# Kernel tuning notes

Measured on AMD Instinct MI355X. Metric: run time of the kernel, lower is better.

## Reference

```python
import jax, jax.numpy as jnp
import numpy as np

N = 4096  # seq len, used for cos/sin positional reweighting


def _non_neg(x):
    # exp(x) for x<0, x+1 for x>=0
    return jnp.where(x < 0, jnp.exp(x), x + 1.0)


def setup_inputs() -> dict:
    key = jax.random.key(0)
    kq, kk, kv = jax.random.split(key, 3)
    shape = (4, 16, N, 64)
    q = jax.random.normal(kq, shape, dtype=jnp.float32)
    k = jax.random.normal(kk, shape, dtype=jnp.float32)
    v = jax.random.normal(kv, shape, dtype=jnp.float32)
    return {"q": q, "k": k, "v": v}


def reference(q, k, v):
    s = q.shape[-2]
    pos = (jnp.pi / 2.0 / s) * jnp.arange(s, dtype=q.dtype)
    cos = jnp.cos(pos)[:, None]  # [S, 1], broadcasts over feature dim
    sin = jnp.sin(pos)[:, None]
    qf = _non_neg(q)
    kf = _non_neg(k)
    q_cos, q_sin = qf * cos, qf * sin  # [B, H, S, D]
    k_cos, k_sin = kf * cos, kf * sin
    # O(N) kv aggregation: [B, H, D, Dv]
    kv_cos = jnp.einsum('bhsd,bhse->bhde', k_cos, v)
    kv_sin = jnp.einsum('bhsd,bhse->bhde', k_sin, v)
    out = jnp.einsum('bhsd,bhde->bhse', q_cos, kv_cos) + \
          jnp.einsum('bhsd,bhde->bhse', q_sin, kv_sin)
    return out
```

## Files before the change

### kernel.cpp

```cpp
#include <hip/hip_runtime.h>
#include <math.h>

#define SLEN 4096
#define DH   64
#define BHN  64
#define CH   16
#define ROWSPER 256
#define NT   4
#define SPAD 72

typedef float  f32x4  __attribute__((ext_vector_type(4)));
typedef short  s16x4  __attribute__((ext_vector_type(4)));
typedef __bf16 bf16x8 __attribute__((ext_vector_type(8)));

static constexpr float ANG  = 1.5707963267948966f / 4096.0f;
static constexpr float C1   = 0.9999999264657180f;
static constexpr float S1   = 3.8349518757139556e-4f;
static constexpr float ROTC = 0.9996988186962042f;
static constexpr float ROTS = 0.024541228522912288f;

static __device__ __forceinline__ float featf(float x) {
    return x < 0.f ? __expf(x) : x + 1.f;
}
static __device__ __forceinline__ void pack2(short* p, float a, float b) {
    union { __bf16 h[2]; unsigned u; } uu;
    uu.h[0] = (__bf16)a; uu.h[1] = (__bf16)b;
    *(unsigned*)p = uu.u;
}
static __device__ __forceinline__ float b2f(short s) {
    unsigned u = ((unsigned)(unsigned short)s) << 16;
    float f; __builtin_memcpy(&f, &u, 4); return f;
}
static __device__ __forceinline__ short f2b(float f) {
    __bf16 h = (__bf16)f; short s; __builtin_memcpy(&s, &h, 2); return s;
}

__global__ __launch_bounds__(256) void kv_partial(const float* __restrict__ k,
                                                  const float* __restrict__ v,
                                                  short* __restrict__ part)
{
    __shared__ short kcT[64 * SPAD];
    __shared__ short ksT[64 * SPAD];
    __shared__ short vT [64 * SPAD];

    const int bx = blockIdx.x;
    const int bh = bx >> 4, ch = bx & 15;
    const size_t base = (size_t)bh * SLEN * DH;
    const int t  = threadIdx.x;
    const int wv = t >> 6;
    const int ln = t & 63;
    const int m  = ln & 15;
    const int g  = ln >> 4;
    const int d0 = (t & 15) * 4;
    const int sg = t >> 4;
    const int srow_base = ch * ROWSPER;

    float cA[2], sA[2], cB[2], sB[2];
    #pragma unroll
    for (int it = 0; it < 2; ++it) {
        float sn, cs;
        __sincosf(ANG * (float)(srow_base + it * 32 + sg * 2), &sn, &cs);
        cA[it] = cs;            sA[it] = sn;
        cB[it] = cs * C1 - sn * S1;
        sB[it] = sn * C1 + cs * S1;
    }

    f32x4 aC[4] = {}; f32x4 aS[4] = {};
    f32x4 K0[2][2], K1[2][2], V0[2][2], V1[2][2];

#define LOADT(BUF, TILE)                                                      \
    _Pragma("unroll")                                                         \
    for (int it = 0; it < 2; ++it) {                                          \
        const size_t r = base + (size_t)(srow_base + (TILE) * 64 + it * 32 + sg * 2) * DH + d0; \
        K0[BUF][it] = *(const f32x4*)&k[r];                                   \
        K1[BUF][it] = *(const f32x4*)&k[r + DH];                              \
        V0[BUF][it] = *(const f32x4*)&v[r];                                   \
        V1[BUF][it] = *(const f32x4*)&v[r + DH];                              \
    }

    LOADT(0, 0);

    #pragma unroll
    for (int tile = 0; tile < NT; ++tile) {
        const int buf = tile & 1;
        if (tile) __syncthreads();
        #pragma unroll
        for (int it = 0; it < 2; ++it) {
            const int sl = it * 32 + sg * 2;
            #pragma unroll
            for (int i = 0; i < 4; ++i) {
                const int d  = d0 + i;
                const float kf0 = featf(K0[buf][it][i]);
                const float kf1 = featf(K1[buf][it][i]);
                const int pos = ((((sl >> 3) ^ ((d >> 2) & 7)) << 3) | (sl & 7));
                const int ro  = d * SPAD + pos;
                pack2(&kcT[ro], kf0 * cA[it], kf1 * cB[it]);
                pack2(&ksT[ro], kf0 * sA[it], kf1 * sB[it]);
                pack2(&vT [ro], V0[buf][it][i], V1[buf][it][i]);
            }
        }
        __syncthreads();
        if (tile + 1 < NT) { LOADT(buf ^ 1, tile + 1); }
        #pragma unroll
        for (int it = 0; it < 2; ++it) {
            float c = cA[it], s = sA[it];
            cA[it] = c * ROTC - s * ROTS; sA[it] = s * ROTC + c * ROTS;
            c = cB[it]; s = sB[it];
            cB[it] = c * ROTC - s * ROTS; sB[it] = s * ROTC + c * ROTS;
        }
        #pragma unroll
        for (int b = 0; b < 2; ++b) {
            const int s3 = b * 4 + g;
            const int dA = wv * 16 + m;
            const int oA = dA * SPAD + ((s3 ^ ((dA >> 2) & 7)) << 3);
            const bf16x8 Ac = *(const bf16x8*)&kcT[oA];
            const bf16x8 As = *(const bf16x8*)&ksT[oA];
            #pragma unroll
            for (int nt = 0; nt < 4; ++nt) {
                const int dB = nt * 16 + m;
                const int oB = dB * SPAD + ((s3 ^ ((dB >> 2) & 7)) << 3);
                const bf16x8 Bv = *(const bf16x8*)&vT[oB];
                aC[nt] = __builtin_amdgcn_mfma_f32_16x16x32_bf16(Ac, Bv, aC[nt], 0, 0, 0);
                aS[nt] = __builtin_amdgcn_mfma_f32_16x16x32_bf16(As, Bv, aS[nt], 0, 0, 0);
            }
        }
    }
#undef LOADT

    const size_t pb = (size_t)bx * 8192;
    #pragma unroll
    for (int nt = 0; nt < 4; ++nt) {
        #pragma unroll
        for (int r = 0; r < 4; ++r) {
            const int rowb = (wv * 16 + g * 4 + r) * 64 + nt * 16 + m;
            part[pb        + rowb] = f2b(aC[nt][r]);
            part[pb + 4096 + rowb] = f2b(aS[nt][r]);
        }
    }
}

__global__ __launch_bounds__(256) void kv_reduce(const short* __restrict__ part,
                                                 short* __restrict__ kvT)
{
    const int bx = blockIdx.x;
    const int bh = bx >> 3, seg = bx & 7;
    const size_t pbase = (size_t)bh * CH * 8192;
    const int j0 = seg * 1024 + threadIdx.x * 4;
    float acc[4] = {};
    #pragma unroll
    for (int c = 0; c < CH; ++c) {
        const s16x4 sv = *(const s16x4*)&part[pbase + (size_t)c * 8192 + j0];
        #pragma unroll
        for (int i = 0; i < 4; ++i) acc[i] += b2f(sv[i]);
    }
    const int cs = j0 >> 12;
    const int d  = (j0 >> 6) & 63;
    const int e0 = j0 & 63;
    #pragma unroll
    for (int i = 0; i < 4; ++i)
        kvT[(size_t)bh * 8192 + cs * 4096 + (e0 + i) * 64 + d] = f2b(acc[i]);
}

__global__ __launch_bounds__(256) void out_kernel(const float* __restrict__ q,
                                                  const short* __restrict__ kvT,
                                                  float* __restrict__ out)
{
    const int bx = blockIdx.x;
    const int bh = bx >> 4, chunk = bx & 15;
    const int t = threadIdx.x;
    const int wv = t >> 6, ln = t & 63, m = ln & 15, g = ln >> 4;
    const size_t qbase = (size_t)bh * SLEN * DH;
    const size_t kvb   = (size_t)bh * 8192;

    bf16x8 Bc[4][2], Bs[4][2];
    #pragma unroll
    for (int nt = 0; nt < 4; ++nt)
        #pragma unroll
        for (int b = 0; b < 2; ++b) {
            const int off = (nt * 16 + m) * 64 + b * 32 + g * 8;
            Bc[nt][b] = *(const bf16x8*)&kvT[kvb + off];
            Bs[nt][b] = *(const bf16x8*)&kvT[kvb + 4096 + off];
        }

    const int sA = chunk * 256 + wv * 16 + m;
    f32x4 qb[4], qn[4];
    #pragma unroll
    for (int p = 0; p < 4; ++p)
        qb[p] = *(const f32x4*)&q[qbase + (size_t)sA * DH + (p >> 1) * 32 + g * 8 + (p & 1) * 4];

    for (int it = 0; it < 4; ++it) {
        const int srow = sA + it * 64;
        if (it < 3) {
            #pragma unroll
            for (int p = 0; p < 4; ++p)
                qn[p] = *(const f32x4*)&q[qbase + (size_t)(srow + 64) * DH + (p >> 1) * 32 + g * 8 + (p & 1) * 4];
        }
        float sn, c;
        __sincosf(ANG * (float)srow, &sn, &c);
        union { bf16x8 v; __bf16 e[8]; } Ac[2], As[2];
        #pragma unroll
        for (int p = 0; p < 4; ++p) {
            #pragma unroll
            for (int i = 0; i < 4; ++i) {
                const float qf = featf(qb[p][i]);
                Ac[p >> 1].e[(p & 1) * 4 + i] = (__bf16)(qf * c);
                As[p >> 1].e[(p & 1) * 4 + i] = (__bf16)(qf * sn);
            }
        }
        f32x4 acc[4] = {};
        #pragma unroll
        for (int nt = 0; nt < 4; ++nt) {
            acc[nt] = __builtin_amdgcn_mfma_f32_16x16x32_bf16(Ac[0].v, Bc[nt][0], acc[nt], 0, 0, 0);
            acc[nt] = __builtin_amdgcn_mfma_f32_16x16x32_bf16(Ac[1].v, Bc[nt][1], acc[nt], 0, 0, 0);
            acc[nt] = __builtin_amdgcn_mfma_f32_16x16x32_bf16(As[0].v, Bs[nt][0], acc[nt], 0, 0, 0);
            acc[nt] = __builtin_amdgcn_mfma_f32_16x16x32_bf16(As[1].v, Bs[nt][1], acc[nt], 0, 0, 0);
        }
        const int s0 = chunk * 256 + (it * 4 + wv) * 16;
        #pragma unroll
        for (int r = 0; r < 4; ++r) {
            const size_t ob = ((size_t)bh * SLEN + s0 + g * 4 + r) * 64;
            #pragma unroll
            for (int nt = 0; nt < 4; ++nt)
                out[ob + nt * 16 + m] = acc[nt][r];
        }
        if (it < 3) {
            #pragma unroll
            for (int p = 0; p < 4; ++p) qb[p] = qn[p];
        }
    }
}

extern "C" void kernel_launch(void* const* d_in, const int* in_sizes, int n_in,
                              void* d_out, int out_size, void* d_ws, size_t ws_size,
                              hipStream_t stream) {
    const float* q = (const float*)d_in[0];
    const float* k = (const float*)d_in[1];
    const float* v = (const float*)d_in[2];
    float* out  = (float*)d_out;
    short* part = (short*)d_ws;
    short* kvT  = (short*)((char*)d_ws + (size_t)BHN * CH * 8192 * 2);

    hipLaunchKernelGGL(kv_partial, dim3(BHN * CH), dim3(256), 0, stream, k, v, part);
    hipLaunchKernelGGL(kv_reduce,  dim3(BHN * 8),  dim3(256), 0, stream, part, kvT);
    hipLaunchKernelGGL(out_kernel, dim3(BHN * 16), dim3(256), 0, stream, q, kvT, out);
}
```

Before: 66.83 us.

## Feed 32x32x16 MFMA operands directly from global loads, dropping LDS staging

The kv_partial kernel no longer transposes K features and V into shared memory. Each lane loads 8 strided scalar rows of k and v straight into registers, builds bf16 MFMA operands in place, and issues 32x32x16 bf16 MFMAs. Each wave covers a 32x32 quadrant of the D x Dv output. The goal is to remove the LDS writes and reads and the block barriers. In exchange, global loads become scalar 4-byte accesses, and each row of k and v is loaded by two waves, which may hurt memory coalescing. Cos/sin are now advanced by a per-step rotation plus small per-row constant tables.

```diff
diff --git a/kernel.cpp b/kernel.cpp
--- a/kernel.cpp
+++ b/kernel.cpp
@@ -6,26 +6,16 @@
 #define BHN  64
 #define CH   16
 #define ROWSPER 256
-#define NT   4
-#define SPAD 72
-
-typedef float  f32x4  __attribute__((ext_vector_type(4)));
-typedef short  s16x4  __attribute__((ext_vector_type(4)));
-typedef __bf16 bf16x8 __attribute__((ext_vector_type(8)));
-
-static constexpr float ANG  = 1.5707963267948966f / 4096.0f;
-static constexpr float C1   = 0.9999999264657180f;
-static constexpr float S1   = 3.8349518757139556e-4f;
-static constexpr float ROTC = 0.9996988186962042f;
-static constexpr float ROTS = 0.024541228522912288f;
+
+typedef float  f32x4   __attribute__((ext_vector_type(4)));
+typedef float  f32x16  __attribute__((ext_vector_type(16)));
+typedef short  s16x4   __attribute__((ext_vector_type(4)));
+typedef __bf16 bf16x8  __attribute__((ext_vector_type(8)));
+
+static constexpr float ANG = 3.8349519697141029e-4f;
 
 static __device__ __forceinline__ float featf(float x) {
     return x < 0.f ? __expf(x) : x + 1.f;
-}
-static __device__ __forceinline__ void pack2(short* p, float a, float b) {
-    union { __bf16 h[2]; unsigned u; } uu;
-    uu.h[0] = (__bf16)a; uu.h[1] = (__bf16)b;
-    *(unsigned*)p = uu.u;
 }
 static __device__ __forceinline__ float b2f(short s) {
     unsigned u = ((unsigned)(unsigned short)s) << 16;
@@ -39,103 +29,73 @@
                                                   const float* __restrict__ v,
                                                   short* __restrict__ part)
 {
-    __shared__ short kcT[64 * SPAD];
-    __shared__ short ksT[64 * SPAD];
-    __shared__ short vT [64 * SPAD];
+    static constexpr float CJ[8] = {
+        1.0f, 0.999999926470f, 0.9999997058633f, 0.9999993381923f,
+        0.9999988234532f, 0.9999981616455f, 0.9999973527695f, 0.9999963968250f};
+    static constexpr float SJ[8] = {
+        0.0f, 3.83495188e-4f, 7.66990319e-4f, 1.15048534e-3f,
+        1.53398019e-3f, 1.91747481e-3f, 2.30096915e-3f, 2.68446316e-3f};
+    static constexpr float RC16 = 0.99998117528260111f;
+    static constexpr float RS16 = 6.1358846491544753e-3f;
 
     const int bx = blockIdx.x;
     const int bh = bx >> 4, ch = bx & 15;
     const size_t base = (size_t)bh * SLEN * DH;
     const int t  = threadIdx.x;
-    const int wv = t >> 6;
-    const int ln = t & 63;
-    const int m  = ln & 15;
-    const int g  = ln >> 4;
-    const int d0 = (t & 15) * 4;
-    const int sg = t >> 4;
-    const int srow_base = ch * ROWSPER;
-
-    float cA[2], sA[2], cB[2], sB[2];
-    #pragma unroll
-    for (int it = 0; it < 2; ++it) {
-        float sn, cs;
-        __sincosf(ANG * (float)(srow_base + it * 32 + sg * 2), &sn, &cs);
-        cA[it] = cs;            sA[it] = sn;
-        cB[it] = cs * C1 - sn * S1;
-        sB[it] = sn * C1 + cs * S1;
-    }
-
-    f32x4 aC[4] = {}; f32x4 aS[4] = {};
-    f32x4 K0[2][2], K1[2][2], V0[2][2], V1[2][2];
-
-#define LOADT(BUF, TILE)                                                      \
-    _Pragma("unroll")                                                         \
-    for (int it = 0; it < 2; ++it) {                                          \
-        const size_t r = base + (size_t)(srow_base + (TILE) * 64 + it * 32 + sg * 2) * DH + d0; \
-        K0[BUF][it] = *(const f32x4*)&k[r];                                   \
-        K1[BUF][it] = *(const f32x4*)&k[r + DH];                              \
-        V0[BUF][it] = *(const f32x4*)&v[r];                                   \
-        V1[BUF][it] = *(const f32x4*)&v[r + DH];                              \
-    }
-
-    LOADT(0, 0);
-
-    #pragma unroll
-    for (int tile = 0; tile < NT; ++tile) {
-        const int buf = tile & 1;
-        if (tile) __syncthreads();
-        #pragma unroll
-        for (int it = 0; it < 2; ++it) {
-            const int sl = it * 32 + sg * 2;
-            #pragma unroll
-            for (int i = 0; i < 4; ++i) {
-                const int d  = d0 + i;
-                const float kf0 = featf(K0[buf][it][i]);
-                const float kf1 = featf(K1[buf][it][i]);
-                const int pos = ((((sl >> 3) ^ ((d >> 2) & 7)) << 3) | (sl & 7));
-                const int ro  = d * SPAD + pos;
-                pack2(&kcT[ro], kf0 * cA[it], kf1 * cB[it]);
-                pack2(&ksT[ro], kf0 * sA[it], kf1 * sB[it]);
-                pack2(&vT [ro], V0[buf][it][i], V1[buf][it][i]);
-            }
-        }
-        __syncthreads();
-        if (tile + 1 < NT) { LOADT(buf ^ 1, tile + 1); }
-        #pragma unroll
-        for (int it = 0; it < 2; ++it) {
-            float c = cA[it], s = sA[it];
-            cA[it] = c * ROTC - s * ROTS; sA[it] = s * ROTC + c * ROTS;
-            c = cB[it]; s = sB[it];
-            cB[it] = c * ROTC - s * ROTS; sB[it] = s * ROTC + c * ROTS;
-        }
-        #pragma unroll
-        for (int b = 0; b < 2; ++b) {
-            const int s3 = b * 4 + g;
-            const int dA = wv * 16 + m;
-            const int oA = dA * SPAD + ((s3 ^ ((dA >> 2) & 7)) << 3);
-            const bf16x8 Ac = *(const bf16x8*)&kcT[oA];
-            const bf16x8 As = *(const bf16x8*)&ksT[oA];
-            #pragma unroll
-            for (int nt = 0; nt < 4; ++nt) {
-                const int dB = nt * 16 + m;
-                const int oB = dB * SPAD + ((s3 ^ ((dB >> 2) & 7)) << 3);
-                const bf16x8 Bv = *(const bf16x8*)&vT[oB];
-                aC[nt] = __builtin_amdgcn_mfma_f32_16x16x32_bf16(Ac, Bv, aC[nt], 0, 0, 0);
-                aS[nt] = __builtin_amdgcn_mfma_f32_16x16x32_bf16(As, Bv, aS[nt], 0, 0, 0);
-            }
-        }
-    }
-#undef LOADT
+    const int w  = t >> 6;
+    const int l  = t & 63;
+    const int m  = l & 31;
+    const int g  = l >> 5;
+    const int dh = w >> 1;
+    const int eh = w & 1;
+    const int dcol = dh * 32 + m;
+    const int ecol = eh * 32 + m;
+    const int s_base = ch * ROWSPER;
+
+    float c0, s0;
+    __sincosf(ANG * (float)(s_base + g * 8), &s0, &c0);
+
+    f32x16 accC = {}; f32x16 accS = {};
+    float kr[2][8], vr[2][8];
+
+#define LOADS(BUF, STEP) {                                                     \
+        const size_t r0 = base + (size_t)(s_base + (STEP) * 16 + g * 8) * DH;  \
+        _Pragma("unroll")                                                      \
+        for (int j = 0; j < 8; ++j) {                                          \
+            kr[BUF][j] = k[r0 + (size_t)j * DH + dcol];                        \
+            vr[BUF][j] = v[r0 + (size_t)j * DH + ecol];                        \
+        } }
+
+    LOADS(0, 0)
+    #pragma unroll
+    for (int step = 0; step < 16; ++step) {
+        const int buf = step & 1;
+        if (step + 1 < 16) LOADS(buf ^ 1, step + 1)
+        union { bf16x8 v; __bf16 e[8]; } Ac, As, Bv;
+        #pragma unroll
+        for (int j = 0; j < 8; ++j) {
+            const float kf = featf(kr[buf][j]);
+            const float p  = kf * c0;
+            const float q  = kf * s0;
+            Ac.e[j] = (__bf16)(p * CJ[j] - q * SJ[j]);
+            As.e[j] = (__bf16)(q * CJ[j] + p * SJ[j]);
+            Bv.e[j] = (__bf16)vr[buf][j];
+        }
+        accC = __builtin_amdgcn_mfma_f32_32x32x16_bf16(Ac.v, Bv.v, accC, 0, 0, 0);
+        accS = __builtin_amdgcn_mfma_f32_32x32x16_bf16(As.v, Bv.v, accS, 0, 0, 0);
+        const float cn = c0 * RC16 - s0 * RS16;
+        s0 = s0 * RC16 + c0 * RS16;
+        c0 = cn;
+    }
+#undef LOADS
 
     const size_t pb = (size_t)bx * 8192;
     #pragma unroll
-    for (int nt = 0; nt < 4; ++nt) {
-        #pragma unroll
-        for (int r = 0; r < 4; ++r) {
-            const int rowb = (wv * 16 + g * 4 + r) * 64 + nt * 16 + m;
-            part[pb        + rowb] = f2b(aC[nt][r]);
-            part[pb + 4096 + rowb] = f2b(aS[nt][r]);
-        }
+    for (int r = 0; r < 16; ++r) {
+        const int drow = dh * 32 + (r & 3) + 8 * (r >> 2) + 4 * g;
+        const size_t o = pb + (size_t)drow * 64 + ecol;
+        part[o]        = f2b(accC[r]);
+        part[o + 4096] = f2b(accS[r]);
     }
 }
 
```

Result: no change. 66.32 us (-0.8%).
